# Kernel tuning notes

Hardware: AMD Instinct MI355X
Metric: run time of the kernel (lower is better)

Reference implementation:

```python
import jax, jax.numpy as jnp
import numpy as np

LN_EPS = 1e-6


def setup_inputs() -> dict:
    key = jax.random.key(0)
    ks = jax.random.split(key, 8)
    B, T, V, r, c, D = 1, 2048, 50257, 16, 16, 1024
    rc = r * c
    return {
        "input_ids": jax.random.randint(ks[0], (B, T), 0, V),
        "token_to_mu_w": jax.random.normal(ks[1], (rc, V), jnp.float32) * 0.02,  # nn.Linear(V, rc).weight
        "pos_embedding": jax.random.normal(ks[2], (1, T, r, c), jnp.float32) * 0.02,
        "w1": jax.random.normal(ks[3], (D, rc), jnp.float32) * 0.05,  # Linear(rc, D).weight
        "b1": jnp.zeros((D,), jnp.float32),
        "ln_w": jnp.ones((D,), jnp.float32),
        "ln_b": jnp.zeros((D,), jnp.float32),
        "w2": jax.random.normal(ks[4], (V, D), jnp.float32) * 0.02,  # Linear(D, V).weight
        "b2": jnp.zeros((V,), jnp.float32),
    }


def reference(input_ids, token_to_mu_w, pos_embedding, w1, b1, ln_w, ln_b, w2, b2):
    B, T = input_ids.shape
    r, c = pos_embedding.shape[2], pos_embedding.shape[3]
    # one_hot(input_ids) @ W^T is exactly a row-gather of W^T (single nonzero per row)
    MU = jnp.take(token_to_mu_w.T, input_ids, axis=0)          # [B, T, rc]
    MU = MU.reshape(B, T, r, c) + pos_embedding[:, :T]         # [B, T, r, c]
    # n_layers = 0: no transformer blocks; dropout is identity in eval
    x = MU.reshape(B, T, r * c)
    h = jax.nn.gelu(jnp.einsum('btk,dk->btd', x, w1) + b1, approximate=False)
    mean = jnp.mean(h, axis=-1, keepdims=True)
    var = jnp.mean(jnp.square(h - mean), axis=-1, keepdims=True)
    h = (h - mean) * jax.lax.rsqrt(var + LN_EPS) * ln_w + ln_b
    logits = jnp.einsum('btd,vd->btv', h, w2) + b2             # [B, T, V]
    return logits, MU
```

## Files before the change

kernel.cpp:

```cpp
#include <hip/hip_runtime.h>
#include <hip/hip_bf16.h>
#include <math.h>

#define T_LEN 2048
#define RC 256
#define DIM 1024
#define VOCAB 50257
#define NT 32
#define SLOT 4096

using short8  = __attribute__((ext_vector_type(8))) short;
using f32x4   = __attribute__((ext_vector_type(4))) float;

#define VMCNT(n) asm volatile("s_waitcnt vmcnt(" #n ")" ::: "memory")
#define SCHED_FENCE() __builtin_amdgcn_sched_barrier(0)

__device__ __forceinline__ unsigned short f2bf(float f) {
    unsigned int u = __float_as_uint(f);
    u += 0x7fffu + ((u >> 16) & 1u);
    return (unsigned short)(u >> 16);
}

__device__ __forceinline__ unsigned int cvt_pk_bf16(float a, float b) {
    unsigned int r;
    asm volatile("v_cvt_pk_bf16_f32 %0, %1, %2" : "=v"(r) : "v"(a), "v"(b));
    return r;
}

__device__ __forceinline__ void async_load16(void* lds, const void* g) {
    __builtin_amdgcn_global_load_lds(
        (const __attribute__((address_space(1))) void*)g,
        (__attribute__((address_space(3))) void*)lds,
        16, 0, 0);
}

__global__ __launch_bounds__(256) void mu_kernel(
    const int* __restrict__ ids, const float* __restrict__ tokw,
    const float* __restrict__ pos, float* __restrict__ mu) {
    int t = blockIdx.x, k = threadIdx.x;
    int id = ids[t];
    float v = tokw[(size_t)k * VOCAB + id] + pos[t * RC + k];
    mu[t * RC + k] = v;
}

__global__ __launch_bounds__(256) void gemm1_gelu_kernel(
    const float* __restrict__ mu, const float* __restrict__ w1,
    const float* __restrict__ b1, float* __restrict__ hpre) {
    __shared__ float xs[16][RC];
    const int tg = blockIdx.x, ng = blockIdx.y, tid = threadIdx.x;
    const int t0 = tg * 16;
    {
        const float4* src = (const float4*)(mu + (size_t)t0 * RC);
        float4* dst = (float4*)&xs[0][0];
        #pragma unroll
        for (int i = 0; i < 4; ++i) dst[tid + 256 * i] = src[tid + 256 * i];
    }
    __syncthreads();
    const int d = ng * 256 + tid;
    float acc[16];
    const float bias = b1[d];
    #pragma unroll
    for (int t = 0; t < 16; ++t) acc[t] = bias;
    const float4* w1r = (const float4*)(w1 + (size_t)d * RC);
    for (int k4 = 0; k4 < RC / 4; ++k4) {
        const float4 w = w1r[k4];
        #pragma unroll
        for (int t = 0; t < 16; ++t) {
            const float4 xv = *(const float4*)&xs[t][k4 * 4];
            acc[t] += w.x * xv.x + w.y * xv.y + w.z * xv.z + w.w * xv.w;
        }
    }
    #pragma unroll
    for (int t = 0; t < 16; ++t) {
        float x = acc[t];
        float g = 0.5f * x * (1.0f + erff(x * 0.70710678118654752f));
        hpre[(size_t)(t0 + t) * DIM + d] = g;
    }
}

__global__ __launch_bounds__(256) void ln_kernel(
    const float* __restrict__ hpre, const float* __restrict__ lnw,
    const float* __restrict__ lnb, unsigned short* __restrict__ h) {
    const int t = blockIdx.x, tid = threadIdx.x;
    const float4 v = ((const float4*)(hpre + (size_t)t * DIM))[tid];
    float s  = v.x + v.y + v.z + v.w;
    float ss = v.x * v.x + v.y * v.y + v.z * v.z + v.w * v.w;
    #pragma unroll
    for (int off = 32; off > 0; off >>= 1) {
        s  += __shfl_down(s, off, 64);
        ss += __shfl_down(ss, off, 64);
    }
    __shared__ float red[8];
    const int wid = tid >> 6, lane = tid & 63;
    if (lane == 0) { red[wid] = s; red[4 + wid] = ss; }
    __syncthreads();
    const float S  = red[0] + red[1] + red[2] + red[3];
    const float SS = red[4] + red[5] + red[6] + red[7];
    const float mean = S * (1.0f / DIM);
    const float var  = SS * (1.0f / DIM) - mean * mean;
    const float inv  = 1.0f / sqrtf(var + 1e-6f);
    const float4 wv = ((const float4*)lnw)[tid];
    const float4 bv = ((const float4*)lnb)[tid];
    ushort4 o;
    o.x = f2bf((v.x - mean) * inv * wv.x + bv.x);
    o.y = f2bf((v.y - mean) * inv * wv.y + bv.y);
    o.z = f2bf((v.z - mean) * inv * wv.z + bv.z);
    o.w = f2bf((v.w - mean) * inv * wv.w + bv.w);
    ((ushort4*)h)[(size_t)t * (DIM / 4) + tid] = o;
}

__global__ __launch_bounds__(256) void cvt_kernel(
    const float* __restrict__ src, unsigned int* __restrict__ dst, int n8) {
    int i = blockIdx.x * 256 + threadIdx.x;
    const int stride = gridDim.x * 256;
    for (; i < n8; i += stride) {
        const float4 a = ((const float4*)src)[2 * i];
        const float4 b = ((const float4*)src)[2 * i + 1];
        uint4 o;
        o.x = cvt_pk_bf16(a.x, a.y);
        o.y = cvt_pk_bf16(a.z, a.w);
        o.z = cvt_pk_bf16(b.x, b.y);
        o.w = cvt_pk_bf16(b.z, b.w);
        ((uint4*)dst)[i] = o;
    }
}

__device__ __forceinline__ void stage_tile(
    const unsigned short* __restrict__ A, const unsigned short* __restrict__ B,
    unsigned short* As_s, unsigned short* Bs_s,
    int m0, int n0, int kt, int tid, int lk_src) {
    #pragma unroll
    for (int p = 0; p < 2; ++p) {
        const int g = p * 256 + tid;
        const int row = g >> 2;
        async_load16(As_s + (size_t)g * 8,
                     A + (size_t)(m0 + row) * DIM + kt * 32 + lk_src * 8);
    }
    #pragma unroll
    for (int p = 0; p < 2; ++p) {
        const int g = p * 256 + tid;
        const int row = g >> 2;
        int bn = n0 + row; if (bn > VOCAB - 1) bn = VOCAB - 1;
        async_load16(Bs_s + (size_t)g * 8,
                     B + (size_t)bn * DIM + kt * 32 + lk_src * 8);
    }
}

__global__ __launch_bounds__(256, 3) void gemm2_kernel(
    const unsigned short* __restrict__ A, const unsigned short* __restrict__ B,
    const float* __restrict__ b2, float* __restrict__ out) {
    __shared__ unsigned short As[3 * SLOT];
    __shared__ unsigned short Bs[3 * SLOT];

    const int tid  = threadIdx.x;
    const int cpx  = gridDim.x >> 3;
    const int wgid = (blockIdx.x & 7) * cpx + (blockIdx.x >> 3);
    const int m0   = (wgid & 15) << 7;
    const int n0   = (wgid >> 4) << 7;

    const int lane = tid & 63;
    const int lr   = lane & 15;
    const int lk   = lane >> 4;
    const int wid  = tid >> 6;
    const int wr   = wid >> 1;
    const int wc   = wid & 1;
    const int xr     = (lk ^ ((lr >> 1) & 3)) * 8;
    const int arow0  = wr * 64 + lr;
    const int brow0  = wc * 64 + lr;
    const int lk_src = (tid & 3) ^ ((tid >> 3) & 3);

    f32x4 acc[4][4];
    #pragma unroll
    for (int m = 0; m < 4; ++m)
        #pragma unroll
        for (int n = 0; n < 4; ++n) acc[m][n] = {0.f, 0.f, 0.f, 0.f};

    stage_tile(A, B, As, Bs, m0, n0, 0, tid, lk_src);
    SCHED_FENCE();
    stage_tile(A, B, As + SLOT, Bs + SLOT, m0, n0, 1, tid, lk_src);
    SCHED_FENCE();
    VMCNT(4);

    int cur = 0, st2 = 2;
    #pragma unroll 1
    for (int t = 0; t < NT; ++t) {
        __builtin_amdgcn_s_barrier();
        SCHED_FENCE();
        const unsigned short* As_t = As + cur * SLOT;
        const unsigned short* Bs_t = Bs + cur * SLOT;
        short8 af[4], bf[4];
        #pragma unroll
        for (int m = 0; m < 4; ++m)
            af[m] = *(const short8*)(As_t + (arow0 + m * 16) * 32 + xr);
        #pragma unroll
        for (int n = 0; n < 4; ++n)
            bf[n] = *(const short8*)(Bs_t + (brow0 + n * 16) * 32 + xr);
        if (t + 2 < NT)
            stage_tile(A, B, As + st2 * SLOT, Bs + st2 * SLOT, m0, n0, t + 2, tid, lk_src);
        SCHED_FENCE();
        if (t < NT - 2) { VMCNT(4); } else { VMCNT(0); }
        __builtin_amdgcn_s_setprio(1);
        #pragma unroll
        for (int m = 0; m < 4; ++m)
            #pragma unroll
            for (int n = 0; n < 4; ++n)
                acc[m][n] = __builtin_amdgcn_mfma_f32_16x16x32_bf16(
                    af[m], bf[n], acc[m][n], 0, 0, 0);
        __builtin_amdgcn_s_setprio(0);
        SCHED_FENCE();
        cur = (cur == 2) ? 0 : cur + 1;
        st2 = (st2 == 2) ? 0 : st2 + 1;
    }

    float bias[4]; int col[4]; bool ok[4];
    #pragma unroll
    for (int n = 0; n < 4; ++n) {
        col[n] = n0 + wc * 64 + n * 16 + lr;
        ok[n]  = col[n] < VOCAB;
        bias[n] = ok[n] ? b2[col[n]] : 0.f;
    }
    #pragma unroll
    for (int m = 0; m < 4; ++m) {
        const int row = m0 + wr * 64 + m * 16 + lk * 4;
        #pragma unroll
        for (int n = 0; n < 4; ++n) {
            if (ok[n]) {
                #pragma unroll
                for (int j = 0; j < 4; ++j)
                    out[(size_t)(row + j) * VOCAB + col[n]] = acc[m][n][j] + bias[n];
            }
        }
    }
}

extern "C" void kernel_launch(void* const* d_in, const int* in_sizes, int n_in,
                              void* d_out, int out_size, void* d_ws, size_t ws_size,
                              hipStream_t stream) {
    (void)in_sizes; (void)n_in; (void)out_size; (void)ws_size;
    const int*   ids  = (const int*)d_in[0];
    const float* tokw = (const float*)d_in[1];
    const float* pos  = (const float*)d_in[2];
    const float* w1   = (const float*)d_in[3];
    const float* b1   = (const float*)d_in[4];
    const float* lnw  = (const float*)d_in[5];
    const float* lnb  = (const float*)d_in[6];
    const float* w2   = (const float*)d_in[7];
    const float* b2   = (const float*)d_in[8];

    float* logits = (float*)d_out;
    float* mu_out = logits + (size_t)T_LEN * VOCAB;

    unsigned short* w2b = (unsigned short*)d_ws;
    unsigned short* hb  = (unsigned short*)((char*)d_ws + (size_t)VOCAB * DIM * 2);
    float* hpre = logits;

    mu_kernel<<<dim3(T_LEN), dim3(256), 0, stream>>>(ids, tokw, pos, mu_out);
    gemm1_gelu_kernel<<<dim3(T_LEN / 16, DIM / 256), dim3(256), 0, stream>>>(
        mu_out, w1, b1, hpre);
    ln_kernel<<<dim3(T_LEN), dim3(256), 0, stream>>>(hpre, lnw, lnb, hb);
    cvt_kernel<<<dim3(2048), dim3(256), 0, stream>>>(
        w2, (unsigned int*)w2b, (int)((size_t)VOCAB * DIM / 8));
    const int ntiles_n = (VOCAB + 127) / 128;
    gemm2_kernel<<<dim3(16 * ntiles_n), dim3(256), 0, stream>>>(hb, w2b, b2, logits);
}
```

Before: 477.1 us.

## Enlarge GEMM2 tile to 256x256 with 8 waves and split-phase pipeline

The logits GEMM moves from 128x128 tiles with 4 waves to 256x256 tiles with 8 waves. Each wave now accumulates an 8x4 grid of MFMA tiles. The K-step is split into two phases that interleave the A and B async loads with the two MFMA halves, separated by extra barriers. This doubles operand reuse per global load and cuts traffic on the large W2 matrix. In exchange it uses more registers and LDS (96KB per block), lowers occupancy, adds barriers, and leaves fewer workgroups, which risks tail imbalance.

```diff
diff --git a/kernel.cpp b/kernel.cpp
--- a/kernel.cpp
+++ b/kernel.cpp
@@ -7,7 +7,7 @@
 #define DIM 1024
 #define VOCAB 50257
 #define NT 32
-#define SLOT 4096
+#define SLOT 8192
 
 using short8  = __attribute__((ext_vector_type(8))) short;
 using f32x4   = __attribute__((ext_vector_type(4))) float;
@@ -125,28 +125,30 @@
     }
 }
 
-__device__ __forceinline__ void stage_tile(
-    const unsigned short* __restrict__ A, const unsigned short* __restrict__ B,
-    unsigned short* As_s, unsigned short* Bs_s,
-    int m0, int n0, int kt, int tid, int lk_src) {
+__device__ __forceinline__ void stage_A512(
+    const unsigned short* __restrict__ A, unsigned short* dst,
+    int m0, int kt, int tid, int gsrc) {
     #pragma unroll
     for (int p = 0; p < 2; ++p) {
-        const int g = p * 256 + tid;
-        const int row = g >> 2;
-        async_load16(As_s + (size_t)g * 8,
-                     A + (size_t)(m0 + row) * DIM + kt * 32 + lk_src * 8);
-    }
+        const int idx = p * 512 + tid;
+        const int row = idx >> 2;
+        async_load16(dst + (size_t)idx * 8,
+                     A + (size_t)(m0 + row) * DIM + kt * 32 + gsrc * 8);
+    }
+}
+__device__ __forceinline__ void stage_B512(
+    const unsigned short* __restrict__ B, unsigned short* dst,
+    int n0, int kt, int tid, int gsrc) {
     #pragma unroll
     for (int p = 0; p < 2; ++p) {
-        const int g = p * 256 + tid;
-        const int row = g >> 2;
-        int bn = n0 + row; if (bn > VOCAB - 1) bn = VOCAB - 1;
-        async_load16(Bs_s + (size_t)g * 8,
-                     B + (size_t)bn * DIM + kt * 32 + lk_src * 8);
-    }
-}
-
-__global__ __launch_bounds__(256, 3) void gemm2_kernel(
+        const int idx = p * 512 + tid;
+        int row = n0 + (idx >> 2); if (row > VOCAB - 1) row = VOCAB - 1;
+        async_load16(dst + (size_t)idx * 8,
+                     B + (size_t)row * DIM + kt * 32 + gsrc * 8);
+    }
+}
+
+__global__ __launch_bounds__(512, 2) void gemm2_kernel(
     const unsigned short* __restrict__ A, const unsigned short* __restrict__ B,
     const float* __restrict__ b2, float* __restrict__ out) {
     __shared__ unsigned short As[3 * SLOT];
@@ -155,40 +157,42 @@
     const int tid  = threadIdx.x;
     const int cpx  = gridDim.x >> 3;
     const int wgid = (blockIdx.x & 7) * cpx + (blockIdx.x >> 3);
-    const int m0   = (wgid & 15) << 7;
-    const int n0   = (wgid >> 4) << 7;
+    const int m0   = (wgid & 7) << 8;
+    const int n0   = (wgid >> 3) << 8;
 
     const int lane = tid & 63;
     const int lr   = lane & 15;
     const int lk   = lane >> 4;
     const int wid  = tid >> 6;
-    const int wr   = wid >> 1;
-    const int wc   = wid & 1;
-    const int xr     = (lk ^ ((lr >> 1) & 3)) * 8;
-    const int arow0  = wr * 64 + lr;
-    const int brow0  = wc * 64 + lr;
-    const int lk_src = (tid & 3) ^ ((tid >> 3) & 3);
-
-    f32x4 acc[4][4];
-    #pragma unroll
-    for (int m = 0; m < 4; ++m)
+    const int wr   = wid >> 2;
+    const int wc   = wid & 3;
+    const int xr   = (lk ^ ((lr >> 1) & 3)) * 8;
+    const int arow0 = wr * 128 + lr;
+    const int brow0 = wc * 64 + lr;
+    const int gsrc = (tid & 3) ^ ((tid >> 3) & 3);
+
+    f32x4 acc[8][4];
+    #pragma unroll
+    for (int m = 0; m < 8; ++m)
         #pragma unroll
         for (int n = 0; n < 4; ++n) acc[m][n] = {0.f, 0.f, 0.f, 0.f};
 
-    stage_tile(A, B, As, Bs, m0, n0, 0, tid, lk_src);
+    stage_A512(A, As, m0, 0, tid, gsrc);
+    stage_B512(B, Bs, n0, 0, tid, gsrc);
     SCHED_FENCE();
-    stage_tile(A, B, As + SLOT, Bs + SLOT, m0, n0, 1, tid, lk_src);
+    stage_A512(A, As + SLOT, m0, 1, tid, gsrc);
+    stage_B512(B, Bs + SLOT, n0, 1, tid, gsrc);
     SCHED_FENCE();
     VMCNT(4);
+    __builtin_amdgcn_s_barrier();
 
     int cur = 0, st2 = 2;
     #pragma unroll 1
     for (int t = 0; t < NT; ++t) {
-        __builtin_amdgcn_s_barrier();
-        SCHED_FENCE();
         const unsigned short* As_t = As + cur * SLOT;
         const unsigned short* Bs_t = Bs + cur * SLOT;
-        short8 af[4], bf[4];
+        short8 af[4], af2[4], bf[4];
+
         #pragma unroll
         for (int m = 0; m < 4; ++m)
             af[m] = *(const short8*)(As_t + (arow0 + m * 16) * 32 + xr);
@@ -196,9 +200,9 @@
         for (int n = 0; n < 4; ++n)
             bf[n] = *(const short8*)(Bs_t + (brow0 + n * 16) * 32 + xr);
         if (t + 2 < NT)
-            stage_tile(A, B, As + st2 * SLOT, Bs + st2 * SLOT, m0, n0, t + 2, tid, lk_src);
-        SCHED_FENCE();
-        if (t < NT - 2) { VMCNT(4); } else { VMCNT(0); }
+            stage_A512(A, As + st2 * SLOT, m0, t + 2, tid, gsrc);
+        SCHED_FENCE();
+        __builtin_amdgcn_s_barrier();
         __builtin_amdgcn_s_setprio(1);
         #pragma unroll
         for (int m = 0; m < 4; ++m)
@@ -208,6 +212,27 @@
                     af[m], bf[n], acc[m][n], 0, 0, 0);
         __builtin_amdgcn_s_setprio(0);
         SCHED_FENCE();
+        __builtin_amdgcn_s_barrier();
+
+        #pragma unroll
+        for (int m = 0; m < 4; ++m)
+            af2[m] = *(const short8*)(As_t + (arow0 + (m + 4) * 16) * 32 + xr);
+        if (t + 2 < NT)
+            stage_B512(B, Bs + st2 * SLOT, n0, t + 2, tid, gsrc);
+        SCHED_FENCE();
+        if (t < NT - 2) { VMCNT(4); } else { VMCNT(0); }
+        __builtin_amdgcn_s_barrier();
+        __builtin_amdgcn_s_setprio(1);
+        #pragma unroll
+        for (int m = 0; m < 4; ++m)
+            #pragma unroll
+            for (int n = 0; n < 4; ++n)
+                acc[m + 4][n] = __builtin_amdgcn_mfma_f32_16x16x32_bf16(
+                    af2[m], bf[n], acc[m + 4][n], 0, 0, 0);
+        __builtin_amdgcn_s_setprio(0);
+        SCHED_FENCE();
+        __builtin_amdgcn_s_barrier();
+
         cur = (cur == 2) ? 0 : cur + 1;
         st2 = (st2 == 2) ? 0 : st2 + 1;
     }
@@ -220,8 +245,8 @@
         bias[n] = ok[n] ? b2[col[n]] : 0.f;
     }
     #pragma unroll
-    for (int m = 0; m < 4; ++m) {
-        const int row = m0 + wr * 64 + m * 16 + lk * 4;
+    for (int m = 0; m < 8; ++m) {
+        const int row = m0 + wr * 128 + m * 16 + lk * 4;
         #pragma unroll
         for (int n = 0; n < 4; ++n) {
             if (ok[n]) {
@@ -260,6 +285,6 @@
     ln_kernel<<<dim3(T_LEN), dim3(256), 0, stream>>>(hpre, lnw, lnb, hb);
     cvt_kernel<<<dim3(2048), dim3(256), 0, stream>>>(
         w2, (unsigned int*)w2b, (int)((size_t)VOCAB * DIM / 8));
-    const int ntiles_n = (VOCAB + 127) / 128;
-    gemm2_kernel<<<dim3(16 * ntiles_n), dim3(256), 0, stream>>>(hb, w2b, b2, logits);
-}
+    const int ntiles_n = (VOCAB + 255) / 256;
+    gemm2_kernel<<<dim3(8 * ntiles_n), dim3(512), 0, stream>>>(hb, w2b, b2, logits);
+}
```

New measurement: 464.2 us, median of 4. 1.03x faster.
